# Kernel tuning notes

Hardware: AMD Instinct MI355X
Metric: run time of the kernel (lower is better)

## Reference

```python
import jax, jax.numpy as jnp
import numpy as np


def setup_inputs() -> dict:
    key = jax.random.key(0)
    k1, k2 = jax.random.split(key)
    B, D, T = 32, 128, 2250
    Q, K = 32, 1024
    embeddings = jax.random.normal(k1, (B, D, T), dtype=jnp.float32)
    embed = jax.random.normal(k2, (Q, K, D), dtype=jnp.float32)
    return {"embeddings": embeddings, "embed": embed}


def reference(embeddings, embed):
    # embeddings: [B, D, T]; embed: [Q, K, D] stacked codebooks.
    B, D, T = embeddings.shape
    Q = embed.shape[0]
    # permute(0,2,1) then flatten, matching EncodecEuclideanCodebook.encode
    x = jnp.transpose(embeddings, (0, 2, 1)).reshape(-1, D)  # [N, D], N = B*T

    def step(residual, e):
        # e: [K, D] codebook for this quantizer layer
        dist = -(jnp.sum(residual * residual, axis=1, keepdims=True)
                 - 2.0 * residual @ e.T
                 + jnp.sum(e * e, axis=1))  # [N, K]
        idx = jnp.argmax(dist, axis=-1)  # [N]
        quantized = e[idx]               # gather [N, D]
        return residual - quantized, idx

    _, indices = jax.lax.scan(step, x, embed)  # indices: [Q, N]
    return indices.reshape(Q, B, T)
```

## Files before the change

### kernel.cpp

```cpp
#include <hip/hip_runtime.h>
#include <hip/hip_bf16.h>

#define B_ 32
#define D_ 128
#define T_ 2250
#define Q_ 32
#define K_ 1024
#define N_ (B_ * T_)
#define TAU 0.25f
#define COFF 640.0f

typedef _Float16 half8 __attribute__((ext_vector_type(8)));
typedef float f32x4 __attribute__((ext_vector_type(4)));

__device__ __forceinline__ unsigned int pack2h(float a, float b) {
    _Float16 ha = (_Float16)a, hb = (_Float16)b;
    unsigned short ua = *(unsigned short*)&ha, ub = *(unsigned short*)&hb;
    return (unsigned int)ua | ((unsigned int)ub << 16);
}

__global__ void transpose_kernel(const float* __restrict__ emb,
                                 double* __restrict__ R64)
{
    __shared__ float tile[32][33];
    const int b  = blockIdx.z;
    const int t0 = blockIdx.x * 32;
    const int d0 = blockIdx.y * 32;

    for (int i = threadIdx.y; i < 32; i += 8) {
        int t = t0 + threadIdx.x;
        int d = d0 + i;
        tile[i][threadIdx.x] = (t < T_) ? emb[((size_t)b * D_ + d) * T_ + t] : 0.0f;
    }
    __syncthreads();
    for (int i = threadIdx.y; i < 32; i += 8) {
        int t = t0 + i;
        if (t < T_) {
            size_t o = ((size_t)b * T_ + t) * D_ + d0 + threadIdx.x;
            R64[o] = (double)tile[threadIdx.x][i];
        }
    }
}

__global__ void cvt_cb_kernel(const float* __restrict__ cbs,
                              _Float16* __restrict__ E16)
{
    int i = blockIdx.x * 256 + threadIdx.x;
    E16[i] = (_Float16)(2.0f * cbs[i]);
}

__global__ __launch_bounds__(64) void norms_kernel(const float* __restrict__ codebooks,
                                                   float* __restrict__ cNorm,
                                                   double* __restrict__ normD)
{
    const int code = blockIdx.x;
    const float* e = codebooks + (size_t)code * D_;
    const int lane = threadIdx.x;
    float f0 = e[lane];
    float f1 = e[lane + 64];
    double acc = (double)f0 * (double)f0 + (double)f1 * (double)f1;
    #pragma unroll
    for (int off = 32; off > 0; off >>= 1) acc += __shfl_down(acc, off);
    if (lane == 0) {
        normD[code] = acc;
        cNorm[code] = COFF - (float)acc;
    }
}

__global__ __launch_bounds__(256) void layer_fast(
    double* __restrict__ R64,
    const int* __restrict__ prevIdx,
    const float* __restrict__ cbPrev,
    const _Float16* __restrict__ E16,
    const float* __restrict__ cNorm,
    int* __restrict__ outIdx,
    int* __restrict__ flagList,
    int* __restrict__ flagCount)
{
    __shared__ __align__(16) char lds[16384];

    const int tid  = threadIdx.x;
    const int lane = tid & 63;
    const int w    = tid >> 6;
    const int mBase = blockIdx.x * 64;

    {
        double2* R64v = (double2*)R64;
        const float2* cbv = (const float2*)cbPrev;
        const int d = lane * 2;
        const int gsh = ((d >> 3) << 4);
        const int bofs = (d & 7) * 2;
        #pragma unroll 8
        for (int k = 0; k < 16; ++k) {
            const int row = k * 4 + w;
            const int grow = mBase + row;
            double2 rv = R64v[(size_t)grow * 64 + lane];
            double rx = rv.x, ry = rv.y;
            if (prevIdx) {
                int code = prevIdx[grow];
                float2 ev = cbv[(size_t)code * 64 + lane];
                rx -= (double)ev.x;
                ry -= (double)ev.y;
                double2 nv; nv.x = rx; nv.y = ry;
                R64v[(size_t)grow * 64 + lane] = nv;
            }
            const int lofs = row * 256 + (gsh ^ ((row & 15) << 4)) + bofs;
            *(unsigned int*)(lds + lofs) = pack2h((float)rx, (float)ry);
        }
    }
    __syncthreads();

    const int l15  = lane & 15;
    const int quad = lane >> 4;

    const int aRowByte = l15 * 256;
    int gofs[4];
    #pragma unroll
    for (int c = 0; c < 4; ++c) gofs[c] = (((c * 4 + quad) ^ l15) << 4);

    const size_t bLane = ((size_t)(w * 32 + l15)) * 256 + (size_t)quad * 16;
    const char* BB = (const char*)E16 + bLane;

    unsigned int b1[16], b2[16];
    #pragma unroll
    for (int s = 0; s < 16; ++s) { b1[s] = 0u; b2[s] = 0u; }

    half8 bc[2];
    #pragma unroll
    for (int j = 0; j < 2; ++j) bc[j] = *(const half8*)(BB + j * 4096);

    #pragma unroll 1
    for (int st = 0; st < 8; ++st) {
        f32x4 acc[4][2];
        #pragma unroll
        for (int i = 0; i < 4; ++i)
            #pragma unroll
            for (int j = 0; j < 2; ++j) acc[i][j] = (f32x4){0.f, 0.f, 0.f, 0.f};

        #pragma unroll
        for (int c = 0; c < 4; ++c) {
            half8 bn[2];
            const bool hn = (c < 3) || (st < 7);
            if (hn) {
                size_t noff = (c < 3) ? ((size_t)st * 32768 + (size_t)(c + 1) * 64)
                                      : ((size_t)(st + 1) * 32768);
                #pragma unroll
                for (int j = 0; j < 2; ++j) bn[j] = *(const half8*)(BB + noff + j * 4096);
            }
            half8 ah[4];
            #pragma unroll
            for (int i = 0; i < 4; ++i)
                ah[i] = *(const half8*)(lds + aRowByte + i * 4096 + gofs[c]);
            #pragma unroll
            for (int i = 0; i < 4; ++i)
                #pragma unroll
                for (int j = 0; j < 2; ++j)
                    acc[i][j] = __builtin_amdgcn_mfma_f32_16x16x32_f16(ah[i], bc[j], acc[i][j], 0, 0, 0);
            if (hn) {
                bc[0] = bn[0]; bc[1] = bn[1];
            }
        }

        #pragma unroll
        for (int j = 0; j < 2; ++j) {
            const int code = st * 128 + w * 32 + j * 16 + l15;
            const float cn = cNorm[code];
            const unsigned int invc = 1023u - (unsigned int)code;
            #pragma unroll
            for (int i = 0; i < 4; ++i)
                #pragma unroll
                for (int r = 0; r < 4; ++r) {
                    float v = fmaxf(acc[i][j][r] + cn, 1.0f);
                    unsigned int p = (__float_as_uint(v) & 0xFFFFFC00u) | invc;
                    const int s = i * 4 + r;
                    unsigned int t  = (b1[s] > p) ? b1[s] : p;
                    unsigned int mn = (b1[s] < p) ? b1[s] : p;
                    b2[s] = (b2[s] > mn) ? b2[s] : mn;
                    b1[s] = t;
                }
        }
    }

    #pragma unroll
    for (int m = 1; m < 16; m <<= 1) {
        #pragma unroll
        for (int s = 0; s < 16; ++s) {
            unsigned int o1 = (unsigned int)__shfl_xor((int)b1[s], m);
            unsigned int o2 = (unsigned int)__shfl_xor((int)b2[s], m);
            unsigned int n1 = (b1[s] > o1) ? b1[s] : o1;
            unsigned int mn = (b1[s] < o1) ? b1[s] : o1;
            unsigned int mx2 = (b2[s] > o2) ? b2[s] : o2;
            b2[s] = (mn > mx2) ? mn : mx2;
            b1[s] = n1;
        }
    }

    __syncthreads();
    unsigned int* m1 = (unsigned int*)lds;
    unsigned int* m2 = (unsigned int*)(lds + 1024);
    if (l15 == 0) {
        #pragma unroll
        for (int i = 0; i < 4; ++i)
            #pragma unroll
            for (int r = 0; r < 4; ++r) {
                int p = i * 16 + quad * 4 + r;
                m1[w * 64 + p] = b1[i * 4 + r];
                m2[w * 64 + p] = b2[i * 4 + r];
            }
    }
    __syncthreads();
    if (tid < 64) {
        unsigned int f1 = m1[tid], f2 = m2[tid];
        #pragma unroll
        for (int ww = 1; ww < 4; ++ww) {
            unsigned int c1 = m1[ww * 64 + tid], c2 = m2[ww * 64 + tid];
            unsigned int mn  = (f1 < c1) ? f1 : c1;
            f1               = (f1 > c1) ? f1 : c1;
            unsigned int mx2 = (f2 > c2) ? f2 : c2;
            f2 = (mn > mx2) ? mn : mx2;
        }
        const int n = mBase + tid;
        outIdx[n] = 1023 - (int)(f1 & 0x3FFu);
        float g1 = __uint_as_float(f1 & 0xFFFFFC00u);
        float g2 = __uint_as_float(f2 & 0xFFFFFC00u);
        if (g1 - g2 < TAU) {
            int pos = atomicAdd(flagCount, 1);
            flagList[pos] = n;
        }
    }
}

#define RPTS 8
__global__ __launch_bounds__(256) void layer_rescore(
    const double* __restrict__ R64,
    const float* __restrict__ cb,
    const double* __restrict__ normD,
    const int* __restrict__ flagList,
    const int* __restrict__ flagCount,
    int* __restrict__ outIdx)
{
    __shared__ __align__(16) double rs[RPTS][D_];
    __shared__ double redS[4][RPTS];
    __shared__ int    redK[4][RPTS];

    const int cnt = *flagCount;
    if (cnt == 0) return;
    const int tid  = threadIdx.x;
    const int lane = tid & 63;
    const int w    = tid >> 6;
    const int nGroups = (cnt + RPTS - 1) / RPTS;

    for (int g = blockIdx.x; g < nGroups; g += gridDim.x) {
        const int base = g * RPTS;
        const int rem  = cnt - base;
        const int npts = (rem < RPTS) ? rem : RPTS;

        __syncthreads();
        for (int i = tid; i < RPTS * D_; i += 256) {
            const int p = i >> 7, j = i & (D_ - 1);
            rs[p][j] = (p < npts) ? R64[(size_t)flagList[base + p] * D_ + j] : 0.0;
        }
        __syncthreads();

        const float* __restrict__ c0 = cb + (size_t)tid * 4 * D_;
        double acc[4][RPTS];
        #pragma unroll
        for (int cc = 0; cc < 4; ++cc)
            #pragma unroll
            for (int p = 0; p < RPTS; ++p) acc[cc][p] = 0.0;

        #pragma unroll 2
        for (int j = 0; j < D_; j += 4) {
            f32x4 cv[4];
            #pragma unroll
            for (int cc = 0; cc < 4; ++cc)
                cv[cc] = *(const f32x4*)(c0 + cc * D_ + j);
            #pragma unroll
            for (int p = 0; p < RPTS; ++p) {
                const double r0 = rs[p][j],     r1 = rs[p][j + 1];
                const double r2 = rs[p][j + 2], r3 = rs[p][j + 3];
                #pragma unroll
                for (int cc = 0; cc < 4; ++cc) {
                    acc[cc][p] = fma((double)cv[cc][0], r0, acc[cc][p]);
                    acc[cc][p] = fma((double)cv[cc][1], r1, acc[cc][p]);
                    acc[cc][p] = fma((double)cv[cc][2], r2, acc[cc][p]);
                    acc[cc][p] = fma((double)cv[cc][3], r3, acc[cc][p]);
                }
            }
        }

        #pragma unroll
        for (int p = 0; p < RPTS; ++p) {
            double bs = -1.0e300;
            int bk = K_;
            #pragma unroll
            for (int cc = 0; cc < 4; ++cc) {
                const int k = tid * 4 + cc;
                double s = 2.0 * acc[cc][p] - normD[k];
                if (s > bs) { bs = s; bk = k; }
            }
            #pragma unroll
            for (int m = 1; m < 64; m <<= 1) {
                double os = __shfl_xor(bs, m);
                int    ok = __shfl_xor(bk, m);
                if (os > bs || (os == bs && ok < bk)) { bs = os; bk = ok; }
            }
            if (lane == 0) { redS[w][p] = bs; redK[w][p] = bk; }
        }
        __syncthreads();
        if (tid < npts) {
            double bs = redS[0][tid];
            int    bk = redK[0][tid];
            #pragma unroll
            for (int ww = 1; ww < 4; ++ww) {
                double s = redS[ww][tid];
                int    k = redK[ww][tid];
                if (s > bs || (s == bs && k < bk)) { bs = s; bk = k; }
            }
            outIdx[flagList[base + tid]] = bk;
        }
    }
}

extern "C" void kernel_launch(void* const* d_in, const int* in_sizes, int n_in,
                              void* d_out, int out_size, void* d_ws, size_t ws_size,
                              hipStream_t stream)
{
    const float* emb       = (const float*)d_in[0];
    const float* codebooks = (const float*)d_in[1];
    int* outIdx = (int*)d_out;

    char* ws = (char*)d_ws;
    double* R64  = (double*)ws;                        size_t off = (size_t)N_ * D_ * 8;
    double* normD = (double*)(ws + off);               off += (size_t)Q_ * K_ * 8;
    _Float16* E16 = (_Float16*)(ws + off);             off += (size_t)Q_ * K_ * D_ * 2;
    float* cNorm    = (float*)(ws + off);              off += (size_t)Q_ * K_ * 4;
    int*   flagList = (int*)(ws + off);                off += (size_t)N_ * 4;
    int*   counters = (int*)(ws + off);                off += (size_t)Q_ * 4;

    hipMemsetAsync(counters, 0, Q_ * 4, stream);

    dim3 tb(32, 8, 1);
    dim3 tg((T_ + 31) / 32, D_ / 32, B_);
    transpose_kernel<<<tg, tb, 0, stream>>>(emb, R64);
    cvt_cb_kernel<<<(Q_ * K_ * D_) / 256, 256, 0, stream>>>(codebooks, E16);
    norms_kernel<<<Q_ * K_, 64, 0, stream>>>(codebooks, cNorm, normD);

    for (int q = 0; q < Q_; ++q) {
        int* oq = outIdx + (size_t)q * N_;
        const int* prevIdx = (q > 0) ? (outIdx + (size_t)(q - 1) * N_) : nullptr;
        const float* cbPrev = codebooks + (size_t)(q > 0 ? q - 1 : 0) * K_ * D_;
        layer_fast<<<N_ / 64, 256, 0, stream>>>(
            R64, prevIdx, cbPrev,
            E16 + (size_t)q * K_ * D_,
            cNorm + (size_t)q * K_, oq, flagList, counters + q);
        layer_rescore<<<1024, 256, 0, stream>>>(
            R64, codebooks + (size_t)q * K_ * D_, normD + (size_t)q * K_,
            flagList, counters + q, oq);
    }
}
```

Baseline: 3.941 ms.

## Store residual in fp32 and recompute exact fp64 residual in rescore

The running residual is now kept in fp32 instead of fp64, which halves the per-layer read/write traffic in layer_fast. To keep the rescore step exact, the rescore kernel rebuilds the fp64 residual for each flagged point from the original input and all previously chosen codes, at a cost of O(q) gathers per point. The codebook prefetch in the MFMA loop is also deepened from one stage to two, with a clamped tail load in place of the conditional. Extra workspace is used for the separate X32 copy of the input.

```diff
diff --git a/kernel.cpp b/kernel.cpp
--- a/kernel.cpp
+++ b/kernel.cpp
@@ -20,7 +20,8 @@
 }
 
 __global__ void transpose_kernel(const float* __restrict__ emb,
-                                 double* __restrict__ R64)
+                                 float* __restrict__ X32,
+                                 float* __restrict__ R32)
 {
     __shared__ float tile[32][33];
     const int b  = blockIdx.z;
@@ -37,7 +38,9 @@
         int t = t0 + i;
         if (t < T_) {
             size_t o = ((size_t)b * T_ + t) * D_ + d0 + threadIdx.x;
-            R64[o] = (double)tile[threadIdx.x][i];
+            float v = tile[threadIdx.x][i];
+            X32[o] = v;
+            R32[o] = v;
         }
     }
 }
@@ -68,7 +71,7 @@
 }
 
 __global__ __launch_bounds__(256) void layer_fast(
-    double* __restrict__ R64,
+    float* __restrict__ R32,
     const int* __restrict__ prevIdx,
     const float* __restrict__ cbPrev,
     const _Float16* __restrict__ E16,
@@ -85,7 +88,7 @@
     const int mBase = blockIdx.x * 64;
 
     {
-        double2* R64v = (double2*)R64;
+        float2* R32v = (float2*)R32;
         const float2* cbv = (const float2*)cbPrev;
         const int d = lane * 2;
         const int gsh = ((d >> 3) << 4);
@@ -94,18 +97,18 @@
         for (int k = 0; k < 16; ++k) {
             const int row = k * 4 + w;
             const int grow = mBase + row;
-            double2 rv = R64v[(size_t)grow * 64 + lane];
-            double rx = rv.x, ry = rv.y;
+            float2 rv = R32v[(size_t)grow * 64 + lane];
+            float rx = rv.x, ry = rv.y;
             if (prevIdx) {
                 int code = prevIdx[grow];
                 float2 ev = cbv[(size_t)code * 64 + lane];
-                rx -= (double)ev.x;
-                ry -= (double)ev.y;
-                double2 nv; nv.x = rx; nv.y = ry;
-                R64v[(size_t)grow * 64 + lane] = nv;
+                rx -= ev.x;
+                ry -= ev.y;
+                float2 nv; nv.x = rx; nv.y = ry;
+                R32v[(size_t)grow * 64 + lane] = nv;
             }
             const int lofs = row * 256 + (gsh ^ ((row & 15) << 4)) + bofs;
-            *(unsigned int*)(lds + lofs) = pack2h((float)rx, (float)ry);
+            *(unsigned int*)(lds + lofs) = pack2h(rx, ry);
         }
     }
     __syncthreads();
@@ -125,9 +128,11 @@
     #pragma unroll
     for (int s = 0; s < 16; ++s) { b1[s] = 0u; b2[s] = 0u; }
 
-    half8 bc[2];
-    #pragma unroll
-    for (int j = 0; j < 2; ++j) bc[j] = *(const half8*)(BB + j * 4096);
+    half8 bc0[2], bc1[2];
+    #pragma unroll
+    for (int j = 0; j < 2; ++j) bc0[j] = *(const half8*)(BB + j * 4096);
+    #pragma unroll
+    for (int j = 0; j < 2; ++j) bc1[j] = *(const half8*)(BB + 64 + j * 4096);
 
     #pragma unroll 1
     for (int st = 0; st < 8; ++st) {
@@ -139,14 +144,13 @@
 
         #pragma unroll
         for (int c = 0; c < 4; ++c) {
+            const int g  = st * 4 + c;
+            const int g2 = (g + 2 < 32) ? g + 2 : 31;
+            const size_t noff = (size_t)(g2 >> 2) * 32768 + (size_t)(g2 & 3) * 64;
             half8 bn[2];
-            const bool hn = (c < 3) || (st < 7);
-            if (hn) {
-                size_t noff = (c < 3) ? ((size_t)st * 32768 + (size_t)(c + 1) * 64)
-                                      : ((size_t)(st + 1) * 32768);
-                #pragma unroll
-                for (int j = 0; j < 2; ++j) bn[j] = *(const half8*)(BB + noff + j * 4096);
-            }
+            #pragma unroll
+            for (int j = 0; j < 2; ++j) bn[j] = *(const half8*)(BB + noff + j * 4096);
+
             half8 ah[4];
             #pragma unroll
             for (int i = 0; i < 4; ++i)
@@ -155,10 +159,9 @@
             for (int i = 0; i < 4; ++i)
                 #pragma unroll
                 for (int j = 0; j < 2; ++j)
-                    acc[i][j] = __builtin_amdgcn_mfma_f32_16x16x32_f16(ah[i], bc[j], acc[i][j], 0, 0, 0);
-            if (hn) {
-                bc[0] = bn[0]; bc[1] = bn[1];
-            }
+                    acc[i][j] = __builtin_amdgcn_mfma_f32_16x16x32_f16(ah[i], bc0[j], acc[i][j], 0, 0, 0);
+            bc0[0] = bc1[0]; bc0[1] = bc1[1];
+            bc1[0] = bn[0];  bc1[1] = bn[1];
         }
 
         #pragma unroll
@@ -232,12 +235,13 @@
 
 #define RPTS 8
 __global__ __launch_bounds__(256) void layer_rescore(
-    const double* __restrict__ R64,
-    const float* __restrict__ cb,
+    const float* __restrict__ X32,
+    const float* __restrict__ cbAll,
     const double* __restrict__ normD,
     const int* __restrict__ flagList,
     const int* __restrict__ flagCount,
-    int* __restrict__ outIdx)
+    int* __restrict__ outIdxAll,
+    const int q)
 {
     __shared__ __align__(16) double rs[RPTS][D_];
     __shared__ double redS[4][RPTS];
@@ -245,9 +249,14 @@
 
     const int cnt = *flagCount;
     if (cnt == 0) return;
+    const float* __restrict__ cb = cbAll + (size_t)q * K_ * D_;
+    int* __restrict__ outIdx = outIdxAll + (size_t)q * N_;
+
     const int tid  = threadIdx.x;
     const int lane = tid & 63;
     const int w    = tid >> 6;
+    const int halfp = tid >> 7;
+    const int jd    = tid & 127;
     const int nGroups = (cnt + RPTS - 1) / RPTS;
 
     for (int g = blockIdx.x; g < nGroups; g += gridDim.x) {
@@ -256,9 +265,21 @@
         const int npts = (rem < RPTS) ? rem : RPTS;
 
         __syncthreads();
-        for (int i = tid; i < RPTS * D_; i += 256) {
-            const int p = i >> 7, j = i & (D_ - 1);
-            rs[p][j] = (p < npts) ? R64[(size_t)flagList[base + p] * D_ + j] : 0.0;
+
+        #pragma unroll 1
+        for (int pp = 0; pp < RPTS; pp += 2) {
+            const int p = pp + halfp;
+            double v = 0.0;
+            if (p < npts) {
+                const int n = flagList[base + p];
+                v = (double)X32[(size_t)n * D_ + jd];
+                #pragma unroll 4
+                for (int qq = 0; qq < q; ++qq) {
+                    const int idx = outIdxAll[(size_t)qq * N_ + n];
+                    v -= (double)cbAll[((size_t)qq * K_ + idx) * D_ + jd];
+                }
+            }
+            rs[p][jd] = v;
         }
         __syncthreads();
 
@@ -331,7 +352,8 @@
     int* outIdx = (int*)d_out;
 
     char* ws = (char*)d_ws;
-    double* R64  = (double*)ws;                        size_t off = (size_t)N_ * D_ * 8;
+    float* X32 = (float*)ws;                           size_t off = (size_t)N_ * D_ * 4;
+    float* R32 = (float*)(ws + off);                   off += (size_t)N_ * D_ * 4;
     double* normD = (double*)(ws + off);               off += (size_t)Q_ * K_ * 8;
     _Float16* E16 = (_Float16*)(ws + off);             off += (size_t)Q_ * K_ * D_ * 2;
     float* cNorm    = (float*)(ws + off);              off += (size_t)Q_ * K_ * 4;
@@ -342,7 +364,7 @@
 
     dim3 tb(32, 8, 1);
     dim3 tg((T_ + 31) / 32, D_ / 32, B_);
-    transpose_kernel<<<tg, tb, 0, stream>>>(emb, R64);
+    transpose_kernel<<<tg, tb, 0, stream>>>(emb, X32, R32);
     cvt_cb_kernel<<<(Q_ * K_ * D_) / 256, 256, 0, stream>>>(codebooks, E16);
     norms_kernel<<<Q_ * K_, 64, 0, stream>>>(codebooks, cNorm, normD);
 
@@ -351,11 +373,11 @@
         const int* prevIdx = (q > 0) ? (outIdx + (size_t)(q - 1) * N_) : nullptr;
         const float* cbPrev = codebooks + (size_t)(q > 0 ? q - 1 : 0) * K_ * D_;
         layer_fast<<<N_ / 64, 256, 0, stream>>>(
-            R64, prevIdx, cbPrev,
+            R32, prevIdx, cbPrev,
             E16 + (size_t)q * K_ * D_,
             cNorm + (size_t)q * K_, oq, flagList, counters + q);
         layer_rescore<<<1024, 256, 0, stream>>>(
-            R64, codebooks + (size_t)q * K_ * D_, normD + (size_t)q * K_,
-            flagList, counters + q, oq);
-    }
-}
+            X32, codebooks, normD + (size_t)q * K_,
+            flagList, counters + q, outIdx, q);
+    }
+}
```

After: 4.451 ms. +12.9%, slower.

## Halve layer_fast row tile, keep A fragments in registers, batch B prefetch

Applied to the files above, without the earlier changes.

Shrinks each block's tile of residual rows from 64 to 32, which doubles the grid and halves LDS use. The A fragments are loaded from LDS into registers once and reused across all codebook stripes. B fragments are now prefetched a whole stripe at a time instead of one chunk at a time, codebook norms are preloaded into registers, and the launch bound asks for 3 blocks per CU. The aim is more occupancy and fewer LDS reads, at the cost of reading the fp16 codebook from global memory twice as often overall.

```diff
diff --git a/kernel.cpp b/kernel.cpp
--- a/kernel.cpp
+++ b/kernel.cpp
@@ -19,6 +19,9 @@
     return (unsigned int)ua | ((unsigned int)ub << 16);
 }
 
+__device__ __forceinline__ unsigned int umax_(unsigned int a, unsigned int b) { return a > b ? a : b; }
+__device__ __forceinline__ unsigned int umin_(unsigned int a, unsigned int b) { return a < b ? a : b; }
+
 __global__ void transpose_kernel(const float* __restrict__ emb,
                                  double* __restrict__ R64)
 {
@@ -67,7 +70,7 @@
     }
 }
 
-__global__ __launch_bounds__(256) void layer_fast(
+__global__ __launch_bounds__(256, 3) void layer_fast(
     double* __restrict__ R64,
     const int* __restrict__ prevIdx,
     const float* __restrict__ cbPrev,
@@ -77,12 +80,32 @@
     int* __restrict__ flagList,
     int* __restrict__ flagCount)
 {
-    __shared__ __align__(16) char lds[16384];
+    __shared__ __align__(16) char lds[8192];
 
     const int tid  = threadIdx.x;
     const int lane = tid & 63;
     const int w    = tid >> 6;
-    const int mBase = blockIdx.x * 64;
+    const int mBase = blockIdx.x * 32;
+
+    const int l15  = lane & 15;
+    const int quad = lane >> 4;
+
+    const size_t bLane = ((size_t)(w * 32 + l15)) * 256 + (size_t)quad * 16;
+    const char* BB = (const char*)E16 + bLane;
+
+    half8 Br[2][4];
+    #pragma unroll
+    for (int j = 0; j < 2; ++j)
+        #pragma unroll
+        for (int c = 0; c < 4; ++c)
+            Br[j][c] = *(const half8*)(BB + (size_t)c * 64 + (size_t)j * 4096);
+
+    float cnr[8][2];
+    #pragma unroll
+    for (int s8 = 0; s8 < 8; ++s8)
+        #pragma unroll
+        for (int j = 0; j < 2; ++j)
+            cnr[s8][j] = cNorm[s8 * 128 + w * 32 + j * 16 + l15];
 
     {
         double2* R64v = (double2*)R64;
@@ -90,8 +113,8 @@
         const int d = lane * 2;
         const int gsh = ((d >> 3) << 4);
         const int bofs = (d & 7) * 2;
-        #pragma unroll 8
-        for (int k = 0; k < 16; ++k) {
+        #pragma unroll
+        for (int k = 0; k < 8; ++k) {
             const int row = k * 4 + w;
             const int grow = mBase + row;
             double2 rv = R64v[(size_t)grow * 64 + lane];
@@ -110,72 +133,59 @@
     }
     __syncthreads();
 
-    const int l15  = lane & 15;
-    const int quad = lane >> 4;
-
-    const int aRowByte = l15 * 256;
-    int gofs[4];
-    #pragma unroll
-    for (int c = 0; c < 4; ++c) gofs[c] = (((c * 4 + quad) ^ l15) << 4);
-
-    const size_t bLane = ((size_t)(w * 32 + l15)) * 256 + (size_t)quad * 16;
-    const char* BB = (const char*)E16 + bLane;
-
-    unsigned int b1[16], b2[16];
-    #pragma unroll
-    for (int s = 0; s < 16; ++s) { b1[s] = 0u; b2[s] = 0u; }
-
-    half8 bc[2];
-    #pragma unroll
-    for (int j = 0; j < 2; ++j) bc[j] = *(const half8*)(BB + j * 4096);
+    half8 a2[4][2];
+    #pragma unroll
+    for (int c = 0; c < 4; ++c) {
+        const int gofs = (((c * 4 + quad) ^ l15) << 4);
+        #pragma unroll
+        for (int i = 0; i < 2; ++i)
+            a2[c][i] = *(const half8*)(lds + l15 * 256 + i * 4096 + gofs);
+    }
+
+    unsigned int b1[8], b2[8];
+    #pragma unroll
+    for (int s = 0; s < 8; ++s) { b1[s] = 0u; b2[s] = 0u; }
 
     #pragma unroll 1
     for (int st = 0; st < 8; ++st) {
-        f32x4 acc[4][2];
-        #pragma unroll
-        for (int i = 0; i < 4; ++i)
+        f32x4 acc[2][2];
+        #pragma unroll
+        for (int i = 0; i < 2; ++i)
             #pragma unroll
             for (int j = 0; j < 2; ++j) acc[i][j] = (f32x4){0.f, 0.f, 0.f, 0.f};
 
         #pragma unroll
-        for (int c = 0; c < 4; ++c) {
-            half8 bn[2];
-            const bool hn = (c < 3) || (st < 7);
-            if (hn) {
-                size_t noff = (c < 3) ? ((size_t)st * 32768 + (size_t)(c + 1) * 64)
-                                      : ((size_t)(st + 1) * 32768);
-                #pragma unroll
-                for (int j = 0; j < 2; ++j) bn[j] = *(const half8*)(BB + noff + j * 4096);
-            }
-            half8 ah[4];
-            #pragma unroll
-            for (int i = 0; i < 4; ++i)
-                ah[i] = *(const half8*)(lds + aRowByte + i * 4096 + gofs[c]);
-            #pragma unroll
-            for (int i = 0; i < 4; ++i)
+        for (int c = 0; c < 4; ++c)
+            #pragma unroll
+            for (int i = 0; i < 2; ++i)
                 #pragma unroll
                 for (int j = 0; j < 2; ++j)
-                    acc[i][j] = __builtin_amdgcn_mfma_f32_16x16x32_f16(ah[i], bc[j], acc[i][j], 0, 0, 0);
-            if (hn) {
-                bc[0] = bn[0]; bc[1] = bn[1];
-            }
+                    acc[i][j] = __builtin_amdgcn_mfma_f32_16x16x32_f16(a2[c][i], Br[j][c], acc[i][j], 0, 0, 0);
+
+        {
+            const size_t soff = (size_t)((st < 7) ? st + 1 : 7) * 32768;
+            #pragma unroll
+            for (int j = 0; j < 2; ++j)
+                #pragma unroll
+                for (int c = 0; c < 4; ++c)
+                    Br[j][c] = *(const half8*)(BB + soff + (size_t)c * 64 + (size_t)j * 4096);
         }
 
         #pragma unroll
         for (int j = 0; j < 2; ++j) {
             const int code = st * 128 + w * 32 + j * 16 + l15;
-            const float cn = cNorm[code];
+            const float cn = cnr[st][j];
             const unsigned int invc = 1023u - (unsigned int)code;
             #pragma unroll
-            for (int i = 0; i < 4; ++i)
+            for (int i = 0; i < 2; ++i)
                 #pragma unroll
                 for (int r = 0; r < 4; ++r) {
                     float v = fmaxf(acc[i][j][r] + cn, 1.0f);
                     unsigned int p = (__float_as_uint(v) & 0xFFFFFC00u) | invc;
                     const int s = i * 4 + r;
-                    unsigned int t  = (b1[s] > p) ? b1[s] : p;
-                    unsigned int mn = (b1[s] < p) ? b1[s] : p;
-                    b2[s] = (b2[s] > mn) ? b2[s] : mn;
+                    unsigned int t  = umax_(b1[s], p);
+                    unsigned int mn = umin_(b1[s], p);
+                    b2[s] = umax_(b2[s], mn);
                     b1[s] = t;
                 }
         }
@@ -184,40 +194,40 @@
     #pragma unroll
     for (int m = 1; m < 16; m <<= 1) {
         #pragma unroll
-        for (int s = 0; s < 16; ++s) {
+        for (int s = 0; s < 8; ++s) {
             unsigned int o1 = (unsigned int)__shfl_xor((int)b1[s], m);
             unsigned int o2 = (unsigned int)__shfl_xor((int)b2[s], m);
-            unsigned int n1 = (b1[s] > o1) ? b1[s] : o1;
-            unsigned int mn = (b1[s] < o1) ? b1[s] : o1;
-            unsigned int mx2 = (b2[s] > o2) ? b2[s] : o2;
-            b2[s] = (mn > mx2) ? mn : mx2;
+            unsigned int n1 = umax_(b1[s], o1);
+            unsigned int mn = umin_(b1[s], o1);
+            unsigned int mx2 = umax_(b2[s], o2);
+            b2[s] = umax_(mn, mx2);
             b1[s] = n1;
         }
     }
 
     __syncthreads();
     unsigned int* m1 = (unsigned int*)lds;
-    unsigned int* m2 = (unsigned int*)(lds + 1024);
+    unsigned int* m2 = (unsigned int*)(lds + 512);
     if (l15 == 0) {
         #pragma unroll
-        for (int i = 0; i < 4; ++i)
+        for (int i = 0; i < 2; ++i)
             #pragma unroll
             for (int r = 0; r < 4; ++r) {
                 int p = i * 16 + quad * 4 + r;
-                m1[w * 64 + p] = b1[i * 4 + r];
-                m2[w * 64 + p] = b2[i * 4 + r];
+                m1[w * 32 + p] = b1[i * 4 + r];
+                m2[w * 32 + p] = b2[i * 4 + r];
             }
     }
     __syncthreads();
-    if (tid < 64) {
+    if (tid < 32) {
         unsigned int f1 = m1[tid], f2 = m2[tid];
         #pragma unroll
         for (int ww = 1; ww < 4; ++ww) {
-            unsigned int c1 = m1[ww * 64 + tid], c2 = m2[ww * 64 + tid];
-            unsigned int mn  = (f1 < c1) ? f1 : c1;
-            f1               = (f1 > c1) ? f1 : c1;
-            unsigned int mx2 = (f2 > c2) ? f2 : c2;
-            f2 = (mn > mx2) ? mn : mx2;
+            unsigned int c1 = m1[ww * 32 + tid], c2 = m2[ww * 32 + tid];
+            unsigned int mn  = umin_(f1, c1);
+            f1               = umax_(f1, c1);
+            unsigned int mx2 = umax_(f2, c2);
+            f2 = umax_(mn, mx2);
         }
         const int n = mBase + tid;
         outIdx[n] = 1023 - (int)(f1 & 0x3FFu);
@@ -350,7 +360,7 @@
         int* oq = outIdx + (size_t)q * N_;
         const int* prevIdx = (q > 0) ? (outIdx + (size_t)(q - 1) * N_) : nullptr;
         const float* cbPrev = codebooks + (size_t)(q > 0 ? q - 1 : 0) * K_ * D_;
-        layer_fast<<<N_ / 64, 256, 0, stream>>>(
+        layer_fast<<<N_ / 32, 256, 0, stream>>>(
             R64, prevIdx, cbPrev,
             E16 + (size_t)q * K_ * D_,
             cNorm + (size_t)q * K_, oq, flagList, counters + q);
```

After: 4.374 ms. 11.0% more time.
